# Kernel tuning notes

Hardware: AMD Instinct MI355X
Metric: run time of the kernel (lower is better)

The kernel has to match this reference:

```python
import jax, jax.numpy as jnp
import numpy as np

WIN_SIZE = 256
PATCH_SIZE = [8]
CHANNEL = 32
B_CH = 256        # B_outer(8) * CHANNEL(32)
H, E = 8, 64


def _attn(q, k):
    # q, k: [B*ch, L, H, E] -> softmax scores [B*ch, H, L, L]
    scale = 1.0 / jnp.sqrt(jnp.asarray(E, q.dtype))
    scores = jnp.einsum('blhe,bshe->bhls', q, k) * scale
    return jax.nn.softmax(scores, axis=-1)  # dropout is identity in eval


def _channel_mean(a):
    # '(b reduce_b) l m n -> b l m n' mean with reduce_b=CHANNEL (channel innermost)
    bc, h, m, n = a.shape
    return a.reshape(bc // CHANNEL, CHANNEL, h, m, n).mean(axis=1)


def setup_inputs() -> dict:
    key = jax.random.key(0)
    k1, k2, k3, k4 = jax.random.split(key, 4)
    p = PATCH_SIZE[0]
    patch_num = WIN_SIZE // p
    return {
        'queries_patch_size': jax.random.normal(k1, (B_CH, patch_num, H, E), jnp.float32),
        'keys_patch_size':    jax.random.normal(k2, (B_CH, patch_num, H, E), jnp.float32),
        'queries_patch_num':  jax.random.normal(k3, (B_CH, p, H, E), jnp.float32),
        'keys_patch_num':     jax.random.normal(k4, (B_CH, p, H, E), jnp.float32),
        'patch_index': 0,
        'attn_mask': 0,
    }


def reference(queries_patch_size, keys_patch_size, queries_patch_num, keys_patch_num, patch_index, attn_mask):
    p = PATCH_SIZE[patch_index]
    rep = WIN_SIZE // p

    # patch_size branch: element-wise repeat (einops repeat) then channel mean.
    # mean over channel commutes with the repeat, so reduce first (same math,
    # avoids the 536MB intermediate the torch code materializes).
    s_ps = _channel_mean(_attn(queries_patch_size, keys_patch_size))  # [B,H,rep,rep]
    s_ps = jnp.repeat(jnp.repeat(s_ps, p, axis=2), p, axis=3)

    # patch_num branch: torch .repeat == tile, then channel mean (also commutes).
    s_pn = _channel_mean(_attn(queries_patch_num, keys_patch_num))    # [B,H,p,p]
    s_pn = jnp.tile(s_pn, (1, 1, rep, rep))

    return (s_ps, s_pn)
```

## Files before the change

kernel.cpp:

```cpp
#include <hip/hip_runtime.h>
#include <stdint.h>


__global__ __launch_bounds__(256, 2)
void scores_kernel(const float* __restrict__ qps,
                   const float* __restrict__ kps,
                   const float* __restrict__ qpn,
                   const float* __restrict__ kpn,
                   float* __restrict__ ws_ps,
                   float* __restrict__ ws_pn)
{
    __shared__ float4 T[4][2][32 * 17];
    const int tid  = threadIdx.x;
    const int wv   = tid >> 6;
    const int lane = tid & 63;
    const int blk  = blockIdx.x;

    if (blk < 512) {
        const int a     = blk >> 3;
        const int chunk = blk & 7;
        const int bo = a >> 3, h = a & 7;
        const int b  = bo * 32 + chunk * 4 + wv;

        const float4* Q4 = reinterpret_cast<const float4*>(qps);
        const float4* K4 = reinterpret_cast<const float4*>(kps);

        const int sr = lane >> 4;
        const int f  = lane & 15;
        float4 qreg[8], kreg[8];
        #pragma unroll
        for (int i = 0; i < 8; ++i) {
            const int row = i * 4 + sr;
            qreg[i] = Q4[((b * 32 + row) * 8 + h) * 16 + f];
            kreg[i] = K4[((b * 32 + row) * 8 + h) * 16 + f];
        }
        #pragma unroll
        for (int i = 0; i < 8; ++i) {
            const int row = i * 4 + sr;
            T[wv][0][row * 17 + f] = qreg[i];
            T[wv][1][row * 17 + f] = kreg[i];
        }

        const int rg = lane >> 3;
        const int cg = lane & 7;

        float acc[4][4];
        #pragma unroll
        for (int r = 0; r < 4; ++r)
            #pragma unroll
            for (int u = 0; u < 4; ++u) acc[r][u] = 0.f;

        #pragma unroll
        for (int c = 0; c < 16; ++c) {
            float4 qv[4], kv[4];
            #pragma unroll
            for (int r = 0; r < 4; ++r) qv[r] = T[wv][0][(rg + 8 * r) * 17 + c];
            #pragma unroll
            for (int u = 0; u < 4; ++u) kv[u] = T[wv][1][(cg + 8 * u) * 17 + c];
            #pragma unroll
            for (int r = 0; r < 4; ++r)
                #pragma unroll
                for (int u = 0; u < 4; ++u) {
                    acc[r][u] = fmaf(qv[r].x, kv[u].x, acc[r][u]);
                    acc[r][u] = fmaf(qv[r].y, kv[u].y, acc[r][u]);
                    acc[r][u] = fmaf(qv[r].z, kv[u].z, acc[r][u]);
                    acc[r][u] = fmaf(qv[r].w, kv[u].w, acc[r][u]);
                }
        }

        #pragma unroll
        for (int r = 0; r < 4; ++r) {
            float v0 = acc[r][0] * 0.125f, v1 = acc[r][1] * 0.125f;
            float v2 = acc[r][2] * 0.125f, v3 = acc[r][3] * 0.125f;
            float m = fmaxf(fmaxf(v0, v1), fmaxf(v2, v3));
            m = fmaxf(m, __shfl_xor(m, 1));
            m = fmaxf(m, __shfl_xor(m, 2));
            m = fmaxf(m, __shfl_xor(m, 4));
            float e0 = __expf(v0 - m), e1 = __expf(v1 - m);
            float e2 = __expf(v2 - m), e3 = __expf(v3 - m);
            float s = (e0 + e1) + (e2 + e3);
            s += __shfl_xor(s, 1);
            s += __shfl_xor(s, 2);
            s += __shfl_xor(s, 4);
            const float inv = 1.f / (s * 32.f);
            acc[r][0] = e0 * inv; acc[r][1] = e1 * inv;
            acc[r][2] = e2 * inv; acc[r][3] = e3 * inv;
        }

        __syncthreads();
        float* P = reinterpret_cast<float*>(T);
        #pragma unroll
        for (int r = 0; r < 4; ++r) {
            const int row = rg + 8 * r;
            const int sw  = (row & 3) << 3;
            #pragma unroll
            for (int u = 0; u < 4; ++u) {
                const int col = cg + 8 * u;
                P[wv * 1024 + row * 32 + (col ^ sw)] = acc[r][u];
            }
        }
        __syncthreads();

        {
            const int row = tid >> 3;
            const int c0  = (tid & 7) * 4;
            const int sw  = (row & 3) << 3;
            float vx[4];
            #pragma unroll
            for (int x = 0; x < 4; ++x) {
                const int ci = row * 32 + ((c0 + x) ^ sw);
                float v = P[ci];
                v += P[1024 + ci];
                v += P[2048 + ci];
                v += P[3072 + ci];
                vx[x] = v;
            }
            float4 o; o.x = vx[0]; o.y = vx[1]; o.z = vx[2]; o.w = vx[3];
            reinterpret_cast<float4*>(ws_ps + (a * 8 + chunk) * 1024)[tid] = o;
        }
    } else {
        float* red = reinterpret_cast<float*>(T);
        const int bb    = blk - 512;
        const int a2    = bb >> 3;
        const int chunk = bb & 7;
        const int bo = a2 >> 3, h = a2 & 7;
        const int b  = bo * 32 + chunk * 4 + wv;
        const int i = lane >> 3, j = lane & 7;
        const float4* qv = reinterpret_cast<const float4*>(qpn) + ((b * 8 + i) * 8 + h) * 16;
        const float4* kv = reinterpret_cast<const float4*>(kpn) + ((b * 8 + j) * 8 + h) * 16;

        float acc = 0.f;
        #pragma unroll
        for (int c = 0; c < 16; ++c) {
            float4 q = qv[c], k = kv[c];
            acc = fmaf(q.x, k.x, acc);
            acc = fmaf(q.y, k.y, acc);
            acc = fmaf(q.z, k.z, acc);
            acc = fmaf(q.w, k.w, acc);
        }
        const float s = acc * 0.125f;
        float m = s;
        m = fmaxf(m, __shfl_xor(m, 1));
        m = fmaxf(m, __shfl_xor(m, 2));
        m = fmaxf(m, __shfl_xor(m, 4));
        float e = __expf(s - m);
        float sum = e;
        sum += __shfl_xor(sum, 1);
        sum += __shfl_xor(sum, 2);
        sum += __shfl_xor(sum, 4);

        red[wv * 64 + lane] = e / (sum * 32.f);
        __syncthreads();
        if (tid < 64) {
            ws_pn[(a2 * 8 + chunk) * 64 + tid] =
                (red[0 * 64 + tid] + red[1 * 64 + tid]) +
                (red[2 * 64 + tid] + red[3 * 64 + tid]);
        }
    }
}

__global__ __launch_bounds__(256)
void writer_kernel(const float* __restrict__ ws_ps,
                   const float* __restrict__ ws_pn,
                   float* __restrict__ out)
{
    const int g = blockIdx.x * 256 + threadIdx.x;
    float4* o4 = reinterpret_cast<float4*>(out);
    if (g < 1048576) {
        const int a  = g >> 14;
        const int r  = g & 16383;
        const int i  = r >> 6;
        const int j4 = r & 63;
        const float* base = ws_ps + a * 8192 + (i >> 3) * 32 + (j4 >> 1);
        float v = 0.f;
        #pragma unroll
        for (int c = 0; c < 8; ++c) v += base[c * 1024];
        float4 o; o.x = v; o.y = v; o.z = v; o.w = v;
        o4[g] = o;
    } else {
        const int g2 = g - 1048576;
        const int a  = g2 >> 14;
        const int r  = g2 & 16383;
        const int i  = r >> 6;
        const int j4 = r & 63;
        const float4* base = reinterpret_cast<const float4*>(
            ws_pn + a * 512 + (i & 7) * 8 + 4 * (j4 & 1));
        float4 v; v.x = 0.f; v.y = 0.f; v.z = 0.f; v.w = 0.f;
        #pragma unroll
        for (int c = 0; c < 8; ++c) {
            float4 t = base[c * 16];
            v.x += t.x; v.y += t.y; v.z += t.z; v.w += t.w;
        }
        o4[g] = v;
    }
}

extern "C" void kernel_launch(void* const* d_in, const int* in_sizes, int n_in,
                              void* d_out, int out_size, void* d_ws, size_t ws_size,
                              hipStream_t stream) {
    const float *qps = nullptr, *kps = nullptr, *qpn = nullptr, *kpn = nullptr;
    for (int idx = 0; idx < n_in; ++idx) {
        if (in_sizes[idx] == 256 * 32 * 8 * 64) {
            if (!qps) qps = (const float*)d_in[idx];
            else if (!kps) kps = (const float*)d_in[idx];
        } else if (in_sizes[idx] == 256 * 8 * 8 * 64) {
            if (!qpn) qpn = (const float*)d_in[idx];
            else if (!kpn) kpn = (const float*)d_in[idx];
        }
    }

    float* ws_ps = (float*)d_ws;
    float* ws_pn = ws_ps + 64 * 8 * 1024;

    scores_kernel<<<1024, 256, 0, stream>>>(qps, kps, qpn, kpn, ws_ps, ws_pn);
    writer_kernel<<<8192, 256, 0, stream>>>(ws_ps, ws_pn, (float*)d_out);
}
```

Before: 108.6 us.

## Split head dim into two LDS halves to shrink shared memory and raise occupancy

The Q/K tile staging in shared memory is split into two halves along the embedding dimension. The second half is held in registers while the first half is consumed from LDS, then it is written into the same LDS slots and consumed. This roughly halves the per-block LDS footprint, and launch bounds are raised to 4 blocks per CU so more waves can hide global-load latency. The global load pattern also changes so that groups of 8 lanes read contiguous 128-byte rows. The cost is more live registers for the staged second half, and register pressure under the tighter launch bound could cause spills.

Measured after the change: 106.1 us. 1.02x faster.

```diff
diff --git a/kernel.cpp b/kernel.cpp
--- a/kernel.cpp
+++ b/kernel.cpp
@@ -2,7 +2,7 @@
 #include <stdint.h>
 
 
-__global__ __launch_bounds__(256, 2)
+__global__ __launch_bounds__(256, 4)
 void scores_kernel(const float* __restrict__ qps,
                    const float* __restrict__ kps,
                    const float* __restrict__ qpn,
@@ -10,7 +10,7 @@
                    float* __restrict__ ws_ps,
                    float* __restrict__ ws_pn)
 {
-    __shared__ float4 T[4][2][32 * 17];
+    __shared__ float4 T[4][2][32 * 9];
     const int tid  = threadIdx.x;
     const int wv   = tid >> 6;
     const int lane = tid & 63;
@@ -25,25 +25,27 @@
         const float4* Q4 = reinterpret_cast<const float4*>(qps);
         const float4* K4 = reinterpret_cast<const float4*>(kps);
 
-        const int sr = lane >> 4;
-        const int f  = lane & 15;
-        float4 qreg[8], kreg[8];
-        #pragma unroll
-        for (int i = 0; i < 8; ++i) {
-            const int row = i * 4 + sr;
-            qreg[i] = Q4[((b * 32 + row) * 8 + h) * 16 + f];
-            kreg[i] = K4[((b * 32 + row) * 8 + h) * 16 + f];
-        }
-        #pragma unroll
-        for (int i = 0; i < 8; ++i) {
-            const int row = i * 4 + sr;
-            T[wv][0][row * 17 + f] = qreg[i];
-            T[wv][1][row * 17 + f] = kreg[i];
-        }
-
         const int rg = lane >> 3;
         const int cg = lane & 7;
 
+        float4 q0[4], k0[4], q1[4], k1[4];
+        #pragma unroll
+        for (int i = 0; i < 4; ++i) {
+            const int row  = 8 * i + rg;
+            const int base = ((b * 32 + row) * 8 + h) * 16;
+            q0[i] = Q4[base + cg];
+            k0[i] = K4[base + cg];
+            q1[i] = Q4[base + 8 + cg];
+            k1[i] = K4[base + 8 + cg];
+        }
+
+        #pragma unroll
+        for (int i = 0; i < 4; ++i) {
+            const int row = 8 * i + rg;
+            T[wv][0][row * 9 + cg] = q0[i];
+            T[wv][1][row * 9 + cg] = k0[i];
+        }
+
         float acc[4][4];
         #pragma unroll
         for (int r = 0; r < 4; ++r)
@@ -51,12 +53,37 @@
             for (int u = 0; u < 4; ++u) acc[r][u] = 0.f;
 
         #pragma unroll
-        for (int c = 0; c < 16; ++c) {
+        for (int c = 0; c < 8; ++c) {
             float4 qv[4], kv[4];
             #pragma unroll
-            for (int r = 0; r < 4; ++r) qv[r] = T[wv][0][(rg + 8 * r) * 17 + c];
-            #pragma unroll
-            for (int u = 0; u < 4; ++u) kv[u] = T[wv][1][(cg + 8 * u) * 17 + c];
+            for (int r = 0; r < 4; ++r) qv[r] = T[wv][0][(rg + 8 * r) * 9 + c];
+            #pragma unroll
+            for (int u = 0; u < 4; ++u) kv[u] = T[wv][1][(cg + 8 * u) * 9 + c];
+            #pragma unroll
+            for (int r = 0; r < 4; ++r)
+                #pragma unroll
+                for (int u = 0; u < 4; ++u) {
+                    acc[r][u] = fmaf(qv[r].x, kv[u].x, acc[r][u]);
+                    acc[r][u] = fmaf(qv[r].y, kv[u].y, acc[r][u]);
+                    acc[r][u] = fmaf(qv[r].z, kv[u].z, acc[r][u]);
+                    acc[r][u] = fmaf(qv[r].w, kv[u].w, acc[r][u]);
+                }
+        }
+
+        #pragma unroll
+        for (int i = 0; i < 4; ++i) {
+            const int row = 8 * i + rg;
+            T[wv][0][row * 9 + cg] = q1[i];
+            T[wv][1][row * 9 + cg] = k1[i];
+        }
+
+        #pragma unroll
+        for (int c = 0; c < 8; ++c) {
+            float4 qv[4], kv[4];
+            #pragma unroll
+            for (int r = 0; r < 4; ++r) qv[r] = T[wv][0][(rg + 8 * r) * 9 + c];
+            #pragma unroll
+            for (int u = 0; u < 4; ++u) kv[u] = T[wv][1][(cg + 8 * u) * 9 + c];
             #pragma unroll
             for (int r = 0; r < 4; ++r)
                 #pragma unroll
```
